# Kernel tuning notes

Measured on AMD Instinct MI355X. Metric: run time of the kernel, lower is better.

## Reference

```python
import jax, jax.numpy as jnp
import numpy as np

NUM_HEADS = 8
SIZES = [(80, 80), (40, 40), (20, 20), (10, 10), (5, 5)]


def _ln(x, g, b):
    m = x.mean(-1, keepdims=True)
    var = ((x - m) ** 2).mean(-1, keepdims=True)
    return (x - m) / jnp.sqrt(var + 1e-5) * g + b


def setup_inputs() -> dict:
    key = jax.random.key(0)
    ks = jax.random.split(key, 24)
    bs, c, S = 2, 256, 1024  # v_dim = embed_dim = c
    d = {}
    for i, (h, w) in enumerate(SIZES):
        d[f"q{i}"] = jax.random.normal(ks[i], (bs, c, h, w), jnp.float32)
    d["cache"] = jax.random.normal(ks[5], (bs, S, c), jnp.float32)
    d["mask"] = jax.random.randint(ks[6], (bs, S), 0, 2).astype(jnp.int32)
    d["ln_v_g"] = jnp.ones((c,), jnp.float32)
    d["ln_v_b"] = jnp.zeros((c,), jnp.float32)
    d["ln_c_g"] = jnp.ones((c,), jnp.float32)
    d["ln_c_b"] = jnp.zeros((c,), jnp.float32)
    sd = c ** -0.5
    d["Wv"] = jax.random.normal(ks[7], (c, c), jnp.float32) * sd
    d["bv"] = jnp.zeros((c,), jnp.float32)
    d["Wc"] = jax.random.normal(ks[8], (c, c), jnp.float32) * sd
    d["bc"] = jnp.zeros((c,), jnp.float32)
    d["Wvc"] = jax.random.normal(ks[9], (c, c), jnp.float32) * sd
    d["bvc"] = jnp.zeros((c,), jnp.float32)
    d["Wo"] = jax.random.normal(ks[10], (c, c), jnp.float32) * sd
    d["bo"] = jnp.zeros((c,), jnp.float32)
    d["Wg1"] = jax.random.normal(ks[11], (c, c // 2), jnp.float32) * sd
    d["bg1"] = jnp.zeros((c // 2,), jnp.float32)
    d["Wg2"] = jax.random.normal(ks[12], (c // 2, c), jnp.float32) * 0.01
    d["bg2"] = jnp.zeros((c,), jnp.float32)
    return d


def _forward(q0, q1, q2, q3, q4, cache, mask, ln_v_g, ln_v_b, ln_c_g, ln_c_b,
             Wv, bv, Wc, bc, Wvc, bvc, Wo, bo, Wg1, bg1, Wg2, bg2):
    feats = [q0, q1, q2, q3, q4]
    bs = q0.shape[0]
    sizes = [(f.shape[2], f.shape[3]) for f in feats]
    # permute_and_flatten: (bs, c, h, w) -> (bs, h*w, c), concat over levels
    v = jnp.concatenate(
        [f.reshape(bs, f.shape[1], -1).transpose(0, 2, 1) for f in feats], axis=1)
    T = v.shape[1]
    E = Wv.shape[1]
    hd = E // NUM_HEADS
    scale = hd ** -0.5

    vn = _ln(v, ln_v_g, ln_v_b)
    cn = _ln(cache, ln_c_g, ln_c_b)

    q = ((vn @ Wv + bv) * scale).reshape(bs, T, NUM_HEADS, hd).transpose(0, 2, 1, 3)
    k = (cn @ Wc + bc).reshape(bs, -1, NUM_HEADS, hd).transpose(0, 2, 1, 3)
    val = (cn @ Wvc + bvc).reshape(bs, -1, NUM_HEADS, hd).transpose(0, 2, 1, 3)

    attn = jnp.einsum('bhtd,bhsd->bhts', q, k)
    attn = jnp.clip(attn, -50000.0, 50000.0)
    mf = mask.astype(attn.dtype)  # (bs, S); zeros -> -9e15, ones kept as +1.0 (faithful)
    attn = attn + jnp.where(mf == 0, jnp.asarray(-9e15, attn.dtype), mf)[:, None, None, :]
    p = jax.nn.softmax(attn, axis=-1)  # dropout inactive in eval mode

    o = jnp.einsum('bhts,bhsd->bhtd', p, val).transpose(0, 2, 1, 3).reshape(bs, T, E)
    delta = o @ Wo + bo

    gate = jnp.tanh(jax.nn.relu(v @ Wg1 + bg1) @ Wg2 + bg2)
    new_v = (v + gate * delta).transpose(0, 2, 1)  # (bs, c, T)

    outs = []
    start = 0
    for h, w in sizes:
        outs.append(new_v[:, :, start:start + h * w].reshape(bs, -1, h, w))
        start += h * w
    return tuple(outs)


def reference(q0, q1, q2, q3, q4, cache, mask, ln_v_g, ln_v_b, ln_c_g, ln_c_b,
              Wv, bv, Wc, bc, Wvc, bvc, Wo, bo, Wg1, bg1, Wg2, bg2):
    return _forward(q0, q1, q2, q3, q4, cache, mask, ln_v_g, ln_v_b, ln_c_g, ln_c_b,
                    Wv, bv, Wc, bc, Wvc, bvc, Wo, bo, Wg1, bg1, Wg2, bg2)
```

## Files before the change

### kernel.cpp

```cpp
#include <hip/hip_runtime.h>
#include <hip/hip_bf16.h>
#include <math.h>


typedef __attribute__((ext_vector_type(8))) short short8;
typedef __attribute__((ext_vector_type(4))) float f32x4;
typedef __hip_bfloat16 bf16;

#define T_TOK 8525
#define S_TOK 1024
#define CDIM  256
#define NHEAD 8
#define BSZ   2

static __device__ __forceinline__ f32x4 mfma16(short8 a, short8 b, f32x4 c) {
  return __builtin_amdgcn_mfma_f32_16x16x32_bf16(a, b, c, 0, 0, 0);
}

static __device__ __forceinline__ float fexp2(float x) {
#if __has_builtin(__builtin_amdgcn_exp2f)
  return __builtin_amdgcn_exp2f(x);
#else
  return exp2f(x);
#endif
}

static __device__ __forceinline__ unsigned int pack_bf16(float a, float b) {
#if __has_builtin(__builtin_amdgcn_perm)
  return __builtin_amdgcn_perm(__float_as_uint(b), __float_as_uint(a), 0x07060302u);
#else
  return (__float_as_uint(a) >> 16) | (__float_as_uint(b) & 0xFFFF0000u);
#endif
}

__global__ __launch_bounds__(256) void stage1(
    const float* __restrict__ q0, const float* __restrict__ q1,
    const float* __restrict__ q2, const float* __restrict__ q3,
    const float* __restrict__ q4,
    const float* __restrict__ Wv, const float* __restrict__ Wc,
    const float* __restrict__ Wvc, const float* __restrict__ Wo,
    const float* __restrict__ Wg1, const float* __restrict__ Wg2,
    const float* __restrict__ bv, const float* __restrict__ bg1,
    const float* __restrict__ bc, const float* __restrict__ bvc,
    const float* __restrict__ cache, const float* __restrict__ ln_c_g,
    const float* __restrict__ ln_c_b, const float* __restrict__ ln_v_g,
    const float* __restrict__ ln_v_b,
    bf16* __restrict__ WqgT, bf16* __restrict__ WcvcT, bf16* __restrict__ WoT,
    bf16* __restrict__ Wg2T, float* __restrict__ biasCV,
    float* __restrict__ biasQG, bf16* __restrict__ cnb,
    float* __restrict__ vT, bf16* __restrict__ vb, bf16* __restrict__ vnb) {
  __shared__ float sm[4160];
  const int bid = blockIdx.x, tid = threadIdx.x;
  if (bid == 80) {
    biasCV[tid] = bc[tid];
    biasCV[tid + 256] = bvc[tid];
    biasQG[tid] = bv[tid];
    if (tid < 128) biasQG[256 + tid] = bg1[tid];
    return;
  }
  if (bid > 80 && bid < 593) {
    int lane = tid & 63;
    int row = (bid - 81) * 4 + (tid >> 6);
    const float* x = cache + (size_t)row * CDIM;
    float v0 = x[lane], v1 = x[lane + 64], v2 = x[lane + 128], v3 = x[lane + 192];
    float s = v0 + v1 + v2 + v3;
    float s2 = v0 * v0 + v1 * v1 + v2 * v2 + v3 * v3;
#pragma unroll
    for (int off = 1; off < 64; off <<= 1) {
      s += __shfl_xor(s, off);
      s2 += __shfl_xor(s2, off);
    }
    float mean = s * (1.f / 256.f);
    float var = s2 * (1.f / 256.f) - mean * mean;
    float rstd = rsqrtf(var + 1e-5f);
    bf16* y = cnb + (size_t)row * CDIM;
    y[lane] = __float2bfloat16((v0 - mean) * rstd * ln_c_g[lane] + ln_c_b[lane]);
    y[lane + 64] = __float2bfloat16((v1 - mean) * rstd * ln_c_g[lane + 64] + ln_c_b[lane + 64]);
    y[lane + 128] = __float2bfloat16((v2 - mean) * rstd * ln_c_g[lane + 128] + ln_c_b[lane + 128]);
    y[lane + 192] = __float2bfloat16((v3 - mean) * rstd * ln_c_g[lane + 192] + ln_c_b[lane + 192]);
    return;
  }
  if (bid < 80) {
    float (*tl)[65] = (float(*)[65])sm;
    const float* W; bf16* WT; int K, N, local;
    if (bid < 16)      { W = Wv;  WT = WqgT;           K = 256; N = 256; local = bid; }
    else if (bid < 32) { W = Wc;  WT = WcvcT;          K = 256; N = 256; local = bid - 16; }
    else if (bid < 48) { W = Wvc; WT = WcvcT + 65536;  K = 256; N = 256; local = bid - 32; }
    else if (bid < 64) { W = Wo;  WT = WoT;            K = 256; N = 256; local = bid - 48; }
    else if (bid < 72) { W = Wg1; WT = WqgT + 65536;   K = 256; N = 128; local = bid - 64; }
    else               { W = Wg2; WT = Wg2T;           K = 128; N = 256; local = bid - 72; }
    const int ktiles = K >> 6;
    const int K0 = (local % ktiles) * 64, N0 = (local / ktiles) * 64;
    const int kk = tid >> 4, n4 = (tid & 15) * 4;
#pragma unroll
    for (int i = 0; i < 4; ++i) {
      int k = kk + 16 * i;
      float4 w4 = *(const float4*)&W[(size_t)(K0 + k) * N + N0 + n4];
      tl[n4 + 0][k] = w4.x; tl[n4 + 1][k] = w4.y;
      tl[n4 + 2][k] = w4.z; tl[n4 + 3][k] = w4.w;
    }
    __syncthreads();
    const int nn = tid >> 4, k4 = (tid & 15) * 4;
#pragma unroll
    for (int i = 0; i < 4; ++i) {
      int n = nn + 16 * i;
      bf16 o[4] __attribute__((aligned(8)));
#pragma unroll
      for (int j = 0; j < 4; ++j) o[j] = __float2bfloat16(tl[n][k4 + j]);
      *(uint2*)&WT[(size_t)(N0 + n) * K + K0 + k4] = *(uint2*)o;
    }
    return;
  }
  constexpr int HW[5] = {6400, 1600, 400, 100, 25};
  constexpr int TST[5] = {0, 6400, 8000, 8400, 8500};
  constexpr int T16[5] = {0, 400, 500, 525, 532};
  float (*tile)[260] = (float(*)[260])sm;
  const int bb = bid - 593;
  const int tileid = bb % 534, b = bb / 534;
  int lvl = 0;
#pragma unroll
  for (int i = 1; i < 5; ++i) if (tileid >= T16[i]) lvl = i;
  const int p0 = (tileid - T16[lvl]) * 16;
  const int hw = HW[lvl];
  const float* src = ((lvl == 0) ? q0 : (lvl == 1) ? q1 : (lvl == 2) ? q2
                      : (lvl == 3) ? q3 : q4) + (size_t)b * CDIM * hw;
  const int pl = tid & 15, cb = tid >> 4;
  const int pg = p0 + pl;
#pragma unroll
  for (int i = 0; i < 16; ++i) {
    int c = cb + 16 * i;
    tile[pl][c] = (pg < hw) ? src[(size_t)c * hw + pg] : 0.f;
  }
  __syncthreads();
  if (pg < hw) {
    int tglob = TST[lvl] + pg;
#pragma unroll
    for (int i = 0; i < 16; ++i) {
      int c = cb + 16 * i;
      vT[((size_t)b * CDIM + c) * T_TOK + tglob] = tile[pl][c];
    }
  }
  const int lane = tid & 63, w = tid >> 6;
#pragma unroll
  for (int rr = 0; rr < 4; ++rr) {
    int row = w * 4 + rr;
    int p = p0 + row;
    if (p >= hw) continue;
    float x0 = tile[row][lane], x1 = tile[row][lane + 64],
          x2 = tile[row][lane + 128], x3 = tile[row][lane + 192];
    float s = x0 + x1 + x2 + x3;
    float s2 = x0 * x0 + x1 * x1 + x2 * x2 + x3 * x3;
#pragma unroll
    for (int off = 1; off < 64; off <<= 1) {
      s += __shfl_xor(s, off);
      s2 += __shfl_xor(s2, off);
    }
    float mean = s * (1.f / 256.f);
    float var = s2 * (1.f / 256.f) - mean * mean;
    float rstd = rsqrtf(var + 1e-5f);
    size_t base = ((size_t)b * T_TOK + TST[lvl] + p) * CDIM;
    float xs[4] = {x0, x1, x2, x3};
#pragma unroll
    for (int j = 0; j < 4; ++j) {
      int c = lane + 64 * j;
      float x = xs[j];
      vb[base + c] = __float2bfloat16(x);
      vnb[base + c] = __float2bfloat16((x - mean) * rstd * ln_v_g[c] + ln_v_b[c]);
    }
  }
}

__global__ __launch_bounds__(256) void gemm_qg(
    const bf16* __restrict__ vnb, const bf16* __restrict__ vb,
    const bf16* __restrict__ WqgT, const float* __restrict__ biasQG,
    bf16* __restrict__ qb, bf16* __restrict__ ghb, int M) {
  __shared__ __align__(16) bf16 Asl[128][136];
  __shared__ __align__(16) bf16 Bsl[64][136];
  const int tid = threadIdx.x;
  const int wave = tid >> 6, lane = tid & 63, quad = lane >> 4, l15 = lane & 15;
  const int m0 = blockIdx.y * 128;
  const int n0 = blockIdx.x * 64;
  const bf16* A = (n0 < 256) ? vnb : vb;
  f32x4 acc[2][4];
#pragma unroll
  for (int i = 0; i < 2; ++i)
#pragma unroll
    for (int j = 0; j < 4; ++j) acc[i][j] = (f32x4){0.f, 0.f, 0.f, 0.f};

  for (int k0 = 0; k0 < 256; k0 += 128) {
    __syncthreads();
#pragma unroll
    for (int c = 0; c < 8; ++c) {
      int chunk = c * 256 + tid;
      int row = chunk >> 4, col = (chunk & 15) * 8;
      int gr = m0 + row;
      if (gr >= M) gr = M - 1;
      *(uint4*)&Asl[row][col] = *(const uint4*)&A[(size_t)gr * 256 + k0 + col];
    }
#pragma unroll
    for (int c = 0; c < 4; ++c) {
      int chunk = c * 256 + tid;
      int row = chunk >> 4, col = (chunk & 15) * 8;
      *(uint4*)&Bsl[row][col] = *(const uint4*)&WqgT[(size_t)(n0 + row) * 256 + k0 + col];
    }
    __syncthreads();
#pragma unroll
    for (int kk = 0; kk < 128; kk += 32) {
      short8 af0 = *(const short8*)&Asl[wave * 32 + l15][kk + quad * 8];
      short8 af1 = *(const short8*)&Asl[wave * 32 + 16 + l15][kk + quad * 8];
      short8 bf0 = *(const short8*)&Bsl[l15][kk + quad * 8];
      short8 bf1 = *(const short8*)&Bsl[16 + l15][kk + quad * 8];
      short8 bf2 = *(const short8*)&Bsl[32 + l15][kk + quad * 8];
      short8 bf3 = *(const short8*)&Bsl[48 + l15][kk + quad * 8];
      acc[0][0] = mfma16(af0, bf0, acc[0][0]);
      acc[0][1] = mfma16(af0, bf1, acc[0][1]);
      acc[0][2] = mfma16(af0, bf2, acc[0][2]);
      acc[0][3] = mfma16(af0, bf3, acc[0][3]);
      acc[1][0] = mfma16(af1, bf0, acc[1][0]);
      acc[1][1] = mfma16(af1, bf1, acc[1][1]);
      acc[1][2] = mfma16(af1, bf2, acc[1][2]);
      acc[1][3] = mfma16(af1, bf3, acc[1][3]);
    }
  }
#pragma unroll
  for (int ms = 0; ms < 2; ++ms)
#pragma unroll
    for (int nt = 0; nt < 4; ++nt)
#pragma unroll
      for (int r = 0; r < 4; ++r) {
        int m = m0 + wave * 32 + ms * 16 + quad * 4 + r;
        if (m >= M) continue;
        int n = n0 + nt * 16 + l15;
        float x = acc[ms][nt][r] + biasQG[n];
        if (n < 256) {
          qb[(size_t)m * 256 + n] = __float2bfloat16(x * 0.25504765517f);
        } else {
          ghb[(size_t)m * 128 + (n - 256)] = __float2bfloat16(fmaxf(x, 0.f));
        }
      }
}

__global__ __launch_bounds__(256) void gemm_kval(
    const bf16* __restrict__ cnb, const bf16* __restrict__ WcvcT,
    const float* __restrict__ biasCV, bf16* __restrict__ kb,
    bf16* __restrict__ valTb, int M) {
  __shared__ __align__(16) bf16 Asl[128][136];
  __shared__ __align__(16) bf16 Bsl[64][136];
  const int tid = threadIdx.x;
  const int wave = tid >> 6, lane = tid & 63, quad = lane >> 4, l15 = lane & 15;
  const int m0 = blockIdx.y * 128;
  const int n0 = blockIdx.x * 64;
  f32x4 acc[2][4];
#pragma unroll
  for (int i = 0; i < 2; ++i)
#pragma unroll
    for (int j = 0; j < 4; ++j) acc[i][j] = (f32x4){0.f, 0.f, 0.f, 0.f};

  for (int k0 = 0; k0 < 256; k0 += 128) {
    __syncthreads();
#pragma unroll
    for (int c = 0; c < 8; ++c) {
      int chunk = c * 256 + tid;
      int row = chunk >> 4, col = (chunk & 15) * 8;
      *(uint4*)&Asl[row][col] = *(const uint4*)&cnb[(size_t)(m0 + row) * 256 + k0 + col];
    }
#pragma unroll
    for (int c = 0; c < 4; ++c) {
      int chunk = c * 256 + tid;
      int row = chunk >> 4, col = (chunk & 15) * 8;
      *(uint4*)&Bsl[row][col] = *(const uint4*)&WcvcT[(size_t)(n0 + row) * 256 + k0 + col];
    }
    __syncthreads();
#pragma unroll
    for (int kk = 0; kk < 128; kk += 32) {
      short8 af0 = *(const short8*)&Asl[wave * 32 + l15][kk + quad * 8];
      short8 af1 = *(const short8*)&Asl[wave * 32 + 16 + l15][kk + quad * 8];
      short8 bf0 = *(const short8*)&Bsl[l15][kk + quad * 8];
      short8 bf1 = *(const short8*)&Bsl[16 + l15][kk + quad * 8];
      short8 bf2 = *(const short8*)&Bsl[32 + l15][kk + quad * 8];
      short8 bf3 = *(const short8*)&Bsl[48 + l15][kk + quad * 8];
      acc[0][0] = mfma16(af0, bf0, acc[0][0]);
      acc[0][1] = mfma16(af0, bf1, acc[0][1]);
      acc[0][2] = mfma16(af0, bf2, acc[0][2]);
      acc[0][3] = mfma16(af0, bf3, acc[0][3]);
      acc[1][0] = mfma16(af1, bf0, acc[1][0]);
      acc[1][1] = mfma16(af1, bf1, acc[1][1]);
      acc[1][2] = mfma16(af1, bf2, acc[1][2]);
      acc[1][3] = mfma16(af1, bf3, acc[1][3]);
    }
  }
#pragma unroll
  for (int ms = 0; ms < 2; ++ms)
#pragma unroll
    for (int nt = 0; nt < 4; ++nt)
#pragma unroll
      for (int r = 0; r < 4; ++r) {
        int m = m0 + wave * 32 + ms * 16 + quad * 4 + r;
        int n = n0 + nt * 16 + l15;
        float x = acc[ms][nt][r] + biasCV[n];
        if (n < 256) {
          kb[(size_t)m * 256 + n] = __float2bfloat16(x);
        } else {
          int n2 = n - 256;
          int bb = m >> 10, s = m & 1023;
          int hh = n2 >> 5, d = n2 & 31;
          valTb[(((size_t)(bb * NHEAD + hh) * 32 + d) << 10) + s] = __float2bfloat16(x);
        }
      }
}

__global__ __launch_bounds__(512) void attn_kernel(
    const bf16* __restrict__ qb, const bf16* __restrict__ kb,
    const bf16* __restrict__ valTb, const int* __restrict__ mask,
    bf16* __restrict__ ob) {
  __shared__ __align__(16) bf16 Ksl[2][4096];
  __shared__ __align__(16) bf16 Vsl[2][4096];
  __shared__ __align__(16) float biasl[2][128];
  const int tid = threadIdx.x;
  const int lane = tid & 63, wv = tid >> 6, quad = lane >> 4, l15 = lane & 15;
  const int b = blockIdx.y >> 3, h = blockIdx.y & 7;
  const int t0w = blockIdx.x * 128 + wv * 16;
  int tA = t0w + l15;
  if (tA >= T_TOK) tA = T_TOK - 1;
  short8 qf = *(const short8*)&qb[((size_t)b * T_TOK + tA) * CDIM + h * 32 + quad * 8];
  f32x4 o0 = {0.f, 0.f, 0.f, 0.f};
  f32x4 o1 = {0.f, 0.f, 0.f, 0.f};
  f32x4 o2 = {0.f, 0.f, 0.f, 0.f};
  const short8 ones = (short8){0x3F80, 0x3F80, 0x3F80, 0x3F80,
                               0x3F80, 0x3F80, 0x3F80, 0x3F80};
  const size_t kbase = ((size_t)b * S_TOK) * CDIM + h * 32;
  const size_t vbase = (size_t)(b * NHEAD + h) << 15;
  const int ks = tid >> 2, kd16 = tid & 3;
  const int kdst = (ks >> 4) * 512 + (ks & 15) * 32 + kd16 * 8;
  const size_t kofs = (size_t)ks * CDIM + kd16 * 8;
  const int vd = tid >> 4, vs8 = (tid & 15) * 8;
  const int schunk = vs8 >> 5, sb_ = vs8 & 31;
  const int kb1 = (((sb_ >> 2) & 3) << 3) + (((sb_ >> 4) & 1) << 2);
  const int sb2_ = sb_ + 4;
  const int kb2 = (((sb2_ >> 2) & 3) << 3) + (((sb2_ >> 4) & 1) << 2);
  const int vbl = schunk * 1024 + (vd >> 4) * 512 + (vd & 15) * 32;
  const int vd1 = vbl + kb1, vd2 = vbl + kb2;
  const size_t vofs = ((size_t)vd << 10) + vs8;

  uint4 kreg = *(const uint4*)&kb[kbase + kofs];
  uint4 vreg = *(const uint4*)&valTb[vbase + vofs];
  float breg = 0.f;
  if (tid < 128) breg = mask[b * S_TOK + tid] ? -12.984255368f : -1e18f;
  *(uint4*)&Ksl[0][kdst] = kreg;
  {
    uint2 lo; lo.x = vreg.x; lo.y = vreg.y;
    uint2 hi; hi.x = vreg.z; hi.y = vreg.w;
    *(uint2*)&Vsl[0][vd1] = lo;
    *(uint2*)&Vsl[0][vd2] = hi;
  }
  if (tid < 128) biasl[0][tid] = breg;
  __syncthreads();

  for (int sbi = 0; sbi < 8; ++sbi) {
    const int cur = sbi & 1;
    if (sbi < 7) {
      int sb = (sbi + 1) * 128;
      kreg = *(const uint4*)&kb[kbase + (size_t)sb * CDIM + kofs];
      vreg = *(const uint4*)&valTb[vbase + sb + vofs];
      if (tid < 128) breg = mask[b * S_TOK + sb + tid] ? -12.984255368f : -1e18f;
    }
#pragma unroll
    for (int ss = 0; ss < 128; ss += 32) {
      const int cb = (ss >> 5) * 1024 + l15 * 32 + quad * 8;
      short8 kf0 = *(const short8*)&Ksl[cur][cb];
      short8 kf1 = *(const short8*)&Ksl[cur][cb + 512];
      short8 vf0 = *(const short8*)&Vsl[cur][cb];
      short8 vf1 = *(const short8*)&Vsl[cur][cb + 512];
      f32x4 bias0 = *(const f32x4*)&biasl[cur][ss + quad * 4];
      f32x4 bias1 = *(const f32x4*)&biasl[cur][ss + 16 + quad * 4];
      f32x4 s0 = mfma16(kf0, qf, bias0);
      f32x4 s1 = mfma16(kf1, qf, bias1);
      float pa = fexp2(s0[0]), pb = fexp2(s0[1]);
      float pc = fexp2(s0[2]), pd = fexp2(s0[3]);
      float pe = fexp2(s1[0]), pf_ = fexp2(s1[1]);
      float pg = fexp2(s1[2]), ph = fexp2(s1[3]);
      uint4 pu;
      pu.x = pack_bf16(pa, pb); pu.y = pack_bf16(pc, pd);
      pu.z = pack_bf16(pe, pf_); pu.w = pack_bf16(pg, ph);
      short8 pfr = *(short8*)&pu;
      o2 = mfma16(pfr, ones, o2);
      o0 = mfma16(pfr, vf0, o0);
      o1 = mfma16(pfr, vf1, o1);
    }
    if (sbi < 7) {
      const int nxt = cur ^ 1;
      *(uint4*)&Ksl[nxt][kdst] = kreg;
      uint2 lo; lo.x = vreg.x; lo.y = vreg.y;
      uint2 hi; hi.x = vreg.z; hi.y = vreg.w;
      *(uint2*)&Vsl[nxt][vd1] = lo;
      *(uint2*)&Vsl[nxt][vd2] = hi;
      if (tid < 128) biasl[nxt][tid] = breg;
    }
    __syncthreads();
  }
  bf16* tile = &Ksl[0][0] + wv * 512;
#pragma unroll
  for (int r = 0; r < 4; ++r) {
    float rli = 1.0f / o2[r];
    int tl = quad * 4 + r;
    tile[tl * 32 + l15] = __float2bfloat16(o0[r] * rli);
    tile[tl * 32 + 16 + l15] = __float2bfloat16(o1[r] * rli);
  }
  {
    int tl = lane >> 2;
    int d8 = (lane & 3) * 8;
    int t = t0w + tl;
    uint4 val = *(const uint4*)&tile[tl * 32 + d8];
    if (t < T_TOK)
      *(uint4*)&ob[((size_t)b * T_TOK + t) * CDIM + h * 32 + d8] = val;
  }
}

__global__ __launch_bounds__(256) void gemm_out(
    const bf16* __restrict__ obuf, const bf16* __restrict__ WoT,
    const float* __restrict__ bo, const bf16* __restrict__ ghb,
    const bf16* __restrict__ Wg2T, const float* __restrict__ bg2,
    const float* __restrict__ vT, float* __restrict__ out, int M) {
  constexpr int HW[5] = {6400, 1600, 400, 100, 25};
  constexpr int TST[5] = {0, 6400, 8000, 8400, 8500};
  constexpr size_t OUTOFF[5] = {0, 3276800, 4096000, 4300800, 4352000};
  __shared__ __align__(16) char smem[52224];
  bf16 (*Asl)[136] = (bf16(*)[136])smem;
  bf16 (*Bsl)[136] = (bf16(*)[136])(smem + 34816);
  float (*tile)[132] = (float(*)[132])smem;
  const int tid = threadIdx.x;
  const int wave = tid >> 6, lane = tid & 63, quad = lane >> 4, l15 = lane & 15;
  const int m0 = blockIdx.y * 128, n0 = blockIdx.x * 64;
  f32x4 aD[2][4], aG[2][4];
#pragma unroll
  for (int i = 0; i < 2; ++i)
#pragma unroll
    for (int j = 0; j < 4; ++j) {
      aD[i][j] = (f32x4){0.f, 0.f, 0.f, 0.f};
      aG[i][j] = (f32x4){0.f, 0.f, 0.f, 0.f};
    }
  for (int k0 = 0; k0 < 256; k0 += 128) {
    __syncthreads();
#pragma unroll
    for (int c = 0; c < 8; ++c) {
      int chunk = c * 256 + tid;
      int row = chunk >> 4, col = (chunk & 15) * 8;
      int gr = m0 + row;
      if (gr >= M) gr = M - 1;
      *(uint4*)&Asl[row][col] = *(const uint4*)&obuf[(size_t)gr * 256 + k0 + col];
    }
#pragma unroll
    for (int c = 0; c < 4; ++c) {
      int chunk = c * 256 + tid;
      int row = chunk >> 4, col = (chunk & 15) * 8;
      *(uint4*)&Bsl[row][col] = *(const uint4*)&WoT[(size_t)(n0 + row) * 256 + k0 + col];
    }
    __syncthreads();
#pragma unroll
    for (int kk = 0; kk < 128; kk += 32) {
      short8 af0 = *(const short8*)&Asl[wave * 32 + l15][kk + quad * 8];
      short8 af1 = *(const short8*)&Asl[wave * 32 + 16 + l15][kk + quad * 8];
#pragma unroll
      for (int j = 0; j < 4; ++j) {
        short8 bfj = *(const short8*)&Bsl[j * 16 + l15][kk + quad * 8];
        aD[0][j] = mfma16(af0, bfj, aD[0][j]);
        aD[1][j] = mfma16(af1, bfj, aD[1][j]);
      }
    }
  }
  __syncthreads();
#pragma unroll
  for (int c = 0; c < 8; ++c) {
    int chunk = c * 256 + tid;
    int row = chunk >> 4, col = (chunk & 15) * 8;
    int gr = m0 + row;
    if (gr >= M) gr = M - 1;
    *(uint4*)&Asl[row][col] = *(const uint4*)&ghb[(size_t)gr * 128 + col];
  }
#pragma unroll
  for (int c = 0; c < 4; ++c) {
    int chunk = c * 256 + tid;
    int row = chunk >> 4, col = (chunk & 15) * 8;
    *(uint4*)&Bsl[row][col] = *(const uint4*)&Wg2T[(size_t)(n0 + row) * 128 + col];
  }
  __syncthreads();
#pragma unroll
  for (int kk = 0; kk < 128; kk += 32) {
    short8 af0 = *(const short8*)&Asl[wave * 32 + l15][kk + quad * 8];
    short8 af1 = *(const short8*)&Asl[wave * 32 + 16 + l15][kk + quad * 8];
#pragma unroll
    for (int j = 0; j < 4; ++j) {
      short8 bfj = *(const short8*)&Bsl[j * 16 + l15][kk + quad * 8];
      aG[0][j] = mfma16(af0, bfj, aG[0][j]);
      aG[1][j] = mfma16(af1, bfj, aG[1][j]);
    }
  }
  __syncthreads();
#pragma unroll
  for (int ms = 0; ms < 2; ++ms)
#pragma unroll
    for (int nt = 0; nt < 4; ++nt) {
      int n = n0 + nt * 16 + l15;
      float bod = bo[n], bgd = bg2[n];
      float4 res;
      float tmp[4];
#pragma unroll
      for (int r = 0; r < 4; ++r) {
        float xd = aD[ms][nt][r] + bod;
        float xg = aG[ms][nt][r] + bgd;
        float xc = fminf(fmaxf(xg, -15.f), 15.f);
        float e = __expf(2.f * xc);
        float gt = (e - 1.f) / (e + 1.f);
        tmp[r] = gt * xd;
      }
      res.x = tmp[0]; res.y = tmp[1]; res.z = tmp[2]; res.w = tmp[3];
      *(float4*)&tile[nt * 16 + l15][wave * 32 + ms * 16 + quad * 4] = res;
    }
  __syncthreads();
  const int tl = tid & 127, c2 = tid >> 7;
  const int t = m0 + tl;
  const bool valid = t < M;
  int bb = (t >= T_TOK) ? 1 : 0;
  int tt = t - bb * T_TOK;
  if (tt >= T_TOK) tt = T_TOK - 1;
  int lvl = 0;
#pragma unroll
  for (int i = 1; i < 5; ++i) if (tt >= TST[i]) lvl = i;
  const int p = tt - TST[lvl], hw = HW[lvl];
  float* dst = out + OUTOFF[lvl] + ((size_t)bb * CDIM + n0) * hw + p;
  const float* vsrc = vT + ((size_t)bb * CDIM + n0) * T_TOK + tt;
#pragma unroll
  for (int c0 = 0; c0 < 32; ++c0) {
    int c = c0 * 2 + c2;
    if (valid) dst[(size_t)c * hw] = vsrc[(size_t)c * T_TOK] + tile[c][tl];
  }
}

extern "C" void kernel_launch(void* const* d_in, const int* in_sizes, int n_in,
                              void* d_out, int out_size, void* d_ws, size_t ws_size,
                              hipStream_t stream) {
  const float* q0 = (const float*)d_in[0];
  const float* q1 = (const float*)d_in[1];
  const float* q2 = (const float*)d_in[2];
  const float* q3 = (const float*)d_in[3];
  const float* q4 = (const float*)d_in[4];
  const float* cache = (const float*)d_in[5];
  const int* mask = (const int*)d_in[6];
  const float* ln_v_g = (const float*)d_in[7];
  const float* ln_v_b = (const float*)d_in[8];
  const float* ln_c_g = (const float*)d_in[9];
  const float* ln_c_b = (const float*)d_in[10];
  const float* Wv = (const float*)d_in[11];
  const float* bv = (const float*)d_in[12];
  const float* Wc = (const float*)d_in[13];
  const float* bc = (const float*)d_in[14];
  const float* Wvc = (const float*)d_in[15];
  const float* bvc = (const float*)d_in[16];
  const float* Wo = (const float*)d_in[17];
  const float* bo = (const float*)d_in[18];
  const float* Wg1 = (const float*)d_in[19];
  const float* bg1 = (const float*)d_in[20];
  const float* Wg2 = (const float*)d_in[21];
  const float* bg2 = (const float*)d_in[22];
  float* out = (float*)d_out;

  const int R = BSZ * T_TOK;
  const size_t RC = (size_t)R * CDIM;
  const size_t SC = (size_t)BSZ * S_TOK * CDIM;

  char* p = (char*)d_ws;
  float* vT = (float*)p;           p += RC * 4;
  bf16* vb = (bf16*)p;             p += RC * 2;
  bf16* vnb = (bf16*)p;            p += RC * 2;
  bf16* qb = (bf16*)p;             p += RC * 2;
  bf16* ob = (bf16*)p;             p += RC * 2;
  bf16* ghb = (bf16*)p;            p += (size_t)R * 128 * 2;
  bf16* cnb = (bf16*)p;            p += SC * 2;
  bf16* kb = (bf16*)p;             p += SC * 2;
  bf16* valTb = (bf16*)p;          p += SC * 2;
  bf16* WqgT = (bf16*)p;           p += 98304 * 2;
  bf16* WcvcT = (bf16*)p;          p += 131072 * 2;
  bf16* WoT = (bf16*)p;            p += 65536 * 2;
  bf16* Wg2T = (bf16*)p;           p += 32768 * 2;
  float* biasCV = (float*)p;       p += 512 * 4;
  float* biasQG = (float*)p;       p += 384 * 4;

  stage1<<<dim3(1661), dim3(256), 0, stream>>>(
      q0, q1, q2, q3, q4, Wv, Wc, Wvc, Wo, Wg1, Wg2, bv, bg1, bc, bvc,
      cache, ln_c_g, ln_c_b, ln_v_g, ln_v_b,
      WqgT, WcvcT, WoT, Wg2T, biasCV, biasQG, cnb, vT, vb, vnb);
  gemm_qg<<<dim3(6, 134), dim3(256), 0, stream>>>(
      vnb, vb, WqgT, biasQG, qb, ghb, R);
  gemm_kval<<<dim3(8, 16), dim3(256), 0, stream>>>(
      cnb, WcvcT, biasCV, kb, valTb, BSZ * S_TOK);
  attn_kernel<<<dim3(67, BSZ * NHEAD), dim3(512), 0, stream>>>(
      qb, kb, valTb, mask, ob);
  gemm_out<<<dim3(4, 134), dim3(256), 0, stream>>>(
      ob, WoT, bo, ghb, Wg2T, bg2, vT, out, R);
}
```

Before: 213.0 us.

## Merge QG and KV GEMMs into one launch, pre-pack mask, store residual as bf16

The two projection GEMMs become a single 1-D grid launch: the first 804 blocks compute Q and the gate hidden layer, the remaining blocks compute K and V. The mask is packed once in stage1 into 16-bit all-ones or zero pairs. The attention kernel now ANDs these masks onto the bf16 probabilities instead of staging a bias row in shared memory and adding it through the MFMA accumulator. The transposed residual copy of v is stored as bf16 rather than fp32, halving its write and read traffic, at the cost of residual precision in the final output. Dropping the constant exponent bias also changes how the exp values are scaled, which could raise overflow risk for large logits.

```diff
diff --git a/kernel.cpp b/kernel.cpp
--- a/kernel.cpp
+++ b/kernel.cpp
@@ -42,13 +42,14 @@
     const float* __restrict__ Wg1, const float* __restrict__ Wg2,
     const float* __restrict__ bv, const float* __restrict__ bg1,
     const float* __restrict__ bc, const float* __restrict__ bvc,
-    const float* __restrict__ cache, const float* __restrict__ ln_c_g,
-    const float* __restrict__ ln_c_b, const float* __restrict__ ln_v_g,
-    const float* __restrict__ ln_v_b,
+    const float* __restrict__ cache, const int* __restrict__ mask,
+    const float* __restrict__ ln_c_g, const float* __restrict__ ln_c_b,
+    const float* __restrict__ ln_v_g, const float* __restrict__ ln_v_b,
     bf16* __restrict__ WqgT, bf16* __restrict__ WcvcT, bf16* __restrict__ WoT,
     bf16* __restrict__ Wg2T, float* __restrict__ biasCV,
-    float* __restrict__ biasQG, bf16* __restrict__ cnb,
-    float* __restrict__ vT, bf16* __restrict__ vb, bf16* __restrict__ vnb) {
+    float* __restrict__ biasQG, unsigned int* __restrict__ mpk,
+    bf16* __restrict__ cnb, bf16* __restrict__ vTb,
+    bf16* __restrict__ vb, bf16* __restrict__ vnb) {
   __shared__ float sm[4160];
   const int bid = blockIdx.x, tid = threadIdx.x;
   if (bid == 80) {
@@ -56,6 +57,12 @@
     biasCV[tid + 256] = bvc[tid];
     biasQG[tid] = bv[tid];
     if (tid < 128) biasQG[256 + tid] = bg1[tid];
+#pragma unroll
+    for (int j = tid; j < 1024; j += 256) {
+      int bb = j >> 9, s2 = (j & 511) * 2;
+      mpk[j] = (mask[bb * 1024 + s2] ? 0xFFFFu : 0u) |
+               (mask[bb * 1024 + s2 + 1] ? 0xFFFF0000u : 0u);
+    }
     return;
   }
   if (bid > 80 && bid < 593) {
@@ -137,7 +144,7 @@
 #pragma unroll
     for (int i = 0; i < 16; ++i) {
       int c = cb + 16 * i;
-      vT[((size_t)b * CDIM + c) * T_TOK + tglob] = tile[pl][c];
+      vTb[((size_t)b * CDIM + c) * T_TOK + tglob] = __float2bfloat16(tile[pl][c]);
     }
   }
   const int lane = tid & 63, w = tid >> 6;
@@ -170,17 +177,30 @@
   }
 }
 
-__global__ __launch_bounds__(256) void gemm_qg(
+__global__ __launch_bounds__(256) void gemm_fused(
     const bf16* __restrict__ vnb, const bf16* __restrict__ vb,
     const bf16* __restrict__ WqgT, const float* __restrict__ biasQG,
-    bf16* __restrict__ qb, bf16* __restrict__ ghb, int M) {
+    bf16* __restrict__ qb, bf16* __restrict__ ghb,
+    const bf16* __restrict__ cnb, const bf16* __restrict__ WcvcT,
+    const float* __restrict__ biasCV, bf16* __restrict__ kb,
+    bf16* __restrict__ valTb) {
   __shared__ __align__(16) bf16 Asl[128][136];
   __shared__ __align__(16) bf16 Bsl[64][136];
   const int tid = threadIdx.x;
   const int wave = tid >> 6, lane = tid & 63, quad = lane >> 4, l15 = lane & 15;
-  const int m0 = blockIdx.y * 128;
-  const int n0 = blockIdx.x * 64;
-  const bf16* A = (n0 < 256) ? vnb : vb;
+  const int bid = blockIdx.x;
+  const bool kval = bid >= 804;
+  int m0, n0, M;
+  const bf16 *A, *BW;
+  const float* bias;
+  if (!kval) {
+    m0 = (bid / 6) * 128; n0 = (bid % 6) * 64;
+    A = (n0 < 256) ? vnb : vb; BW = WqgT; bias = biasQG; M = BSZ * T_TOK;
+  } else {
+    int i = bid - 804;
+    m0 = (i / 8) * 128; n0 = (i % 8) * 64;
+    A = cnb; BW = WcvcT; bias = biasCV; M = BSZ * S_TOK;
+  }
   f32x4 acc[2][4];
 #pragma unroll
   for (int i = 0; i < 2; ++i)
@@ -201,7 +221,7 @@
     for (int c = 0; c < 4; ++c) {
       int chunk = c * 256 + tid;
       int row = chunk >> 4, col = (chunk & 15) * 8;
-      *(uint4*)&Bsl[row][col] = *(const uint4*)&WqgT[(size_t)(n0 + row) * 256 + k0 + col];
+      *(uint4*)&Bsl[row][col] = *(const uint4*)&BW[(size_t)(n0 + row) * 256 + k0 + col];
     }
     __syncthreads();
 #pragma unroll
@@ -231,91 +251,32 @@
         int m = m0 + wave * 32 + ms * 16 + quad * 4 + r;
         if (m >= M) continue;
         int n = n0 + nt * 16 + l15;
-        float x = acc[ms][nt][r] + biasQG[n];
-        if (n < 256) {
-          qb[(size_t)m * 256 + n] = __float2bfloat16(x * 0.25504765517f);
+        float x = acc[ms][nt][r] + bias[n];
+        if (!kval) {
+          if (n < 256) {
+            qb[(size_t)m * 256 + n] = __float2bfloat16(x * 0.25504765517f);
+          } else {
+            ghb[(size_t)m * 128 + (n - 256)] = __float2bfloat16(fmaxf(x, 0.f));
+          }
         } else {
-          ghb[(size_t)m * 128 + (n - 256)] = __float2bfloat16(fmaxf(x, 0.f));
+          if (n < 256) {
+            kb[(size_t)m * 256 + n] = __float2bfloat16(x);
+          } else {
+            int n2 = n - 256;
+            int bb = m >> 10, s = m & 1023;
+            int hh = n2 >> 5, d = n2 & 31;
+            valTb[(((size_t)(bb * NHEAD + hh) * 32 + d) << 10) + s] = __float2bfloat16(x);
+          }
         }
       }
 }
 
-__global__ __launch_bounds__(256) void gemm_kval(
-    const bf16* __restrict__ cnb, const bf16* __restrict__ WcvcT,
-    const float* __restrict__ biasCV, bf16* __restrict__ kb,
-    bf16* __restrict__ valTb, int M) {
-  __shared__ __align__(16) bf16 Asl[128][136];
-  __shared__ __align__(16) bf16 Bsl[64][136];
-  const int tid = threadIdx.x;
-  const int wave = tid >> 6, lane = tid & 63, quad = lane >> 4, l15 = lane & 15;
-  const int m0 = blockIdx.y * 128;
-  const int n0 = blockIdx.x * 64;
-  f32x4 acc[2][4];
-#pragma unroll
-  for (int i = 0; i < 2; ++i)
-#pragma unroll
-    for (int j = 0; j < 4; ++j) acc[i][j] = (f32x4){0.f, 0.f, 0.f, 0.f};
-
-  for (int k0 = 0; k0 < 256; k0 += 128) {
-    __syncthreads();
-#pragma unroll
-    for (int c = 0; c < 8; ++c) {
-      int chunk = c * 256 + tid;
-      int row = chunk >> 4, col = (chunk & 15) * 8;
-      *(uint4*)&Asl[row][col] = *(const uint4*)&cnb[(size_t)(m0 + row) * 256 + k0 + col];
-    }
-#pragma unroll
-    for (int c = 0; c < 4; ++c) {
-      int chunk = c * 256 + tid;
-      int row = chunk >> 4, col = (chunk & 15) * 8;
-      *(uint4*)&Bsl[row][col] = *(const uint4*)&WcvcT[(size_t)(n0 + row) * 256 + k0 + col];
-    }
-    __syncthreads();
-#pragma unroll
-    for (int kk = 0; kk < 128; kk += 32) {
-      short8 af0 = *(const short8*)&Asl[wave * 32 + l15][kk + quad * 8];
-      short8 af1 = *(const short8*)&Asl[wave * 32 + 16 + l15][kk + quad * 8];
-      short8 bf0 = *(const short8*)&Bsl[l15][kk + quad * 8];
-      short8 bf1 = *(const short8*)&Bsl[16 + l15][kk + quad * 8];
-      short8 bf2 = *(const short8*)&Bsl[32 + l15][kk + quad * 8];
-      short8 bf3 = *(const short8*)&Bsl[48 + l15][kk + quad * 8];
-      acc[0][0] = mfma16(af0, bf0, acc[0][0]);
-      acc[0][1] = mfma16(af0, bf1, acc[0][1]);
-      acc[0][2] = mfma16(af0, bf2, acc[0][2]);
-      acc[0][3] = mfma16(af0, bf3, acc[0][3]);
-      acc[1][0] = mfma16(af1, bf0, acc[1][0]);
-      acc[1][1] = mfma16(af1, bf1, acc[1][1]);
-      acc[1][2] = mfma16(af1, bf2, acc[1][2]);
-      acc[1][3] = mfma16(af1, bf3, acc[1][3]);
-    }
-  }
-#pragma unroll
-  for (int ms = 0; ms < 2; ++ms)
-#pragma unroll
-    for (int nt = 0; nt < 4; ++nt)
-#pragma unroll
-      for (int r = 0; r < 4; ++r) {
-        int m = m0 + wave * 32 + ms * 16 + quad * 4 + r;
-        int n = n0 + nt * 16 + l15;
-        float x = acc[ms][nt][r] + biasCV[n];
-        if (n < 256) {
-          kb[(size_t)m * 256 + n] = __float2bfloat16(x);
-        } else {
-          int n2 = n - 256;
-          int bb = m >> 10, s = m & 1023;
-          int hh = n2 >> 5, d = n2 & 31;
-          valTb[(((size_t)(bb * NHEAD + hh) * 32 + d) << 10) + s] = __float2bfloat16(x);
-        }
-      }
-}
-
 __global__ __launch_bounds__(512) void attn_kernel(
     const bf16* __restrict__ qb, const bf16* __restrict__ kb,
-    const bf16* __restrict__ valTb, const int* __restrict__ mask,
+    const bf16* __restrict__ valTb, const unsigned int* __restrict__ mpk,
     bf16* __restrict__ ob) {
   __shared__ __align__(16) bf16 Ksl[2][4096];
   __shared__ __align__(16) bf16 Vsl[2][4096];
-  __shared__ __align__(16) float biasl[2][128];
   const int tid = threadIdx.x;
   const int lane = tid & 63, wv = tid >> 6, quad = lane >> 4, l15 = lane & 15;
   const int b = blockIdx.y >> 3, h = blockIdx.y & 7;
@@ -326,10 +287,12 @@
   f32x4 o0 = {0.f, 0.f, 0.f, 0.f};
   f32x4 o1 = {0.f, 0.f, 0.f, 0.f};
   f32x4 o2 = {0.f, 0.f, 0.f, 0.f};
+  const f32x4 zero4 = {0.f, 0.f, 0.f, 0.f};
   const short8 ones = (short8){0x3F80, 0x3F80, 0x3F80, 0x3F80,
                                0x3F80, 0x3F80, 0x3F80, 0x3F80};
   const size_t kbase = ((size_t)b * S_TOK) * CDIM + h * 32;
   const size_t vbase = (size_t)(b * NHEAD + h) << 15;
+  const unsigned int* mrow = mpk + b * 512;
   const int ks = tid >> 2, kd16 = tid & 3;
   const int kdst = (ks >> 4) * 512 + (ks & 15) * 32 + kd16 * 8;
   const size_t kofs = (size_t)ks * CDIM + kd16 * 8;
@@ -344,8 +307,6 @@
 
   uint4 kreg = *(const uint4*)&kb[kbase + kofs];
   uint4 vreg = *(const uint4*)&valTb[vbase + vofs];
-  float breg = 0.f;
-  if (tid < 128) breg = mask[b * S_TOK + tid] ? -12.984255368f : -1e18f;
   *(uint4*)&Ksl[0][kdst] = kreg;
   {
     uint2 lo; lo.x = vreg.x; lo.y = vreg.y;
@@ -353,7 +314,6 @@
     *(uint2*)&Vsl[0][vd1] = lo;
     *(uint2*)&Vsl[0][vd2] = hi;
   }
-  if (tid < 128) biasl[0][tid] = breg;
   __syncthreads();
 
   for (int sbi = 0; sbi < 8; ++sbi) {
@@ -362,8 +322,8 @@
       int sb = (sbi + 1) * 128;
       kreg = *(const uint4*)&kb[kbase + (size_t)sb * CDIM + kofs];
       vreg = *(const uint4*)&valTb[vbase + sb + vofs];
-      if (tid < 128) breg = mask[b * S_TOK + sb + tid] ? -12.984255368f : -1e18f;
-    }
+    }
+    const unsigned int* mchunk = mrow + sbi * 64;
 #pragma unroll
     for (int ss = 0; ss < 128; ss += 32) {
       const int cb = (ss >> 5) * 1024 + l15 * 32 + quad * 8;
@@ -371,17 +331,19 @@
       short8 kf1 = *(const short8*)&Ksl[cur][cb + 512];
       short8 vf0 = *(const short8*)&Vsl[cur][cb];
       short8 vf1 = *(const short8*)&Vsl[cur][cb + 512];
-      f32x4 bias0 = *(const f32x4*)&biasl[cur][ss + quad * 4];
-      f32x4 bias1 = *(const f32x4*)&biasl[cur][ss + 16 + quad * 4];
-      f32x4 s0 = mfma16(kf0, qf, bias0);
-      f32x4 s1 = mfma16(kf1, qf, bias1);
+      uint2 mk0 = *(const uint2*)&mchunk[(ss >> 1) + quad * 2];
+      uint2 mk1 = *(const uint2*)&mchunk[(ss >> 1) + 8 + quad * 2];
+      f32x4 s0 = mfma16(kf0, qf, zero4);
+      f32x4 s1 = mfma16(kf1, qf, zero4);
       float pa = fexp2(s0[0]), pb = fexp2(s0[1]);
       float pc = fexp2(s0[2]), pd = fexp2(s0[3]);
       float pe = fexp2(s1[0]), pf_ = fexp2(s1[1]);
       float pg = fexp2(s1[2]), ph = fexp2(s1[3]);
       uint4 pu;
-      pu.x = pack_bf16(pa, pb); pu.y = pack_bf16(pc, pd);
-      pu.z = pack_bf16(pe, pf_); pu.w = pack_bf16(pg, ph);
+      pu.x = pack_bf16(pa, pb) & mk0.x;
+      pu.y = pack_bf16(pc, pd) & mk0.y;
+      pu.z = pack_bf16(pe, pf_) & mk1.x;
+      pu.w = pack_bf16(pg, ph) & mk1.y;
       short8 pfr = *(short8*)&pu;
       o2 = mfma16(pfr, ones, o2);
       o0 = mfma16(pfr, vf0, o0);
@@ -394,7 +356,6 @@
       uint2 hi; hi.x = vreg.z; hi.y = vreg.w;
       *(uint2*)&Vsl[nxt][vd1] = lo;
       *(uint2*)&Vsl[nxt][vd2] = hi;
-      if (tid < 128) biasl[nxt][tid] = breg;
     }
     __syncthreads();
   }
@@ -420,7 +381,7 @@
     const bf16* __restrict__ obuf, const bf16* __restrict__ WoT,
     const float* __restrict__ bo, const bf16* __restrict__ ghb,
     const bf16* __restrict__ Wg2T, const float* __restrict__ bg2,
-    const float* __restrict__ vT, float* __restrict__ out, int M) {
+    const bf16* __restrict__ vTb, float* __restrict__ out, int M) {
   constexpr int HW[5] = {6400, 1600, 400, 100, 25};
   constexpr int TST[5] = {0, 6400, 8000, 8400, 8500};
   constexpr size_t OUTOFF[5] = {0, 3276800, 4096000, 4300800, 4352000};
@@ -528,11 +489,12 @@
   for (int i = 1; i < 5; ++i) if (tt >= TST[i]) lvl = i;
   const int p = tt - TST[lvl], hw = HW[lvl];
   float* dst = out + OUTOFF[lvl] + ((size_t)bb * CDIM + n0) * hw + p;
-  const float* vsrc = vT + ((size_t)bb * CDIM + n0) * T_TOK + tt;
+  const bf16* vsrc = vTb + ((size_t)bb * CDIM + n0) * T_TOK + tt;
 #pragma unroll
   for (int c0 = 0; c0 < 32; ++c0) {
     int c = c0 * 2 + c2;
-    if (valid) dst[(size_t)c * hw] = vsrc[(size_t)c * T_TOK] + tile[c][tl];
+    if (valid)
+      dst[(size_t)c * hw] = __bfloat162float(vsrc[(size_t)c * T_TOK]) + tile[c][tl];
   }
 }
 
@@ -569,7 +531,7 @@
   const size_t SC = (size_t)BSZ * S_TOK * CDIM;
 
   char* p = (char*)d_ws;
-  float* vT = (float*)p;           p += RC * 4;
+  bf16* vTb = (bf16*)p;            p += RC * 2;
   bf16* vb = (bf16*)p;             p += RC * 2;
   bf16* vnb = (bf16*)p;            p += RC * 2;
   bf16* qb = (bf16*)p;             p += RC * 2;
@@ -584,17 +546,16 @@
   bf16* Wg2T = (bf16*)p;           p += 32768 * 2;
   float* biasCV = (float*)p;       p += 512 * 4;
   float* biasQG = (float*)p;       p += 384 * 4;
+  unsigned int* mpk = (unsigned int*)p; p += 1024 * 4;
 
   stage1<<<dim3(1661), dim3(256), 0, stream>>>(
       q0, q1, q2, q3, q4, Wv, Wc, Wvc, Wo, Wg1, Wg2, bv, bg1, bc, bvc,
-      cache, ln_c_g, ln_c_b, ln_v_g, ln_v_b,
-      WqgT, WcvcT, WoT, Wg2T, biasCV, biasQG, cnb, vT, vb, vnb);
-  gemm_qg<<<dim3(6, 134), dim3(256), 0, stream>>>(
-      vnb, vb, WqgT, biasQG, qb, ghb, R);
-  gemm_kval<<<dim3(8, 16), dim3(256), 0, stream>>>(
-      cnb, WcvcT, biasCV, kb, valTb, BSZ * S_TOK);
+      cache, mask, ln_c_g, ln_c_b, ln_v_g, ln_v_b,
+      WqgT, WcvcT, WoT, Wg2T, biasCV, biasQG, mpk, cnb, vTb, vb, vnb);
+  gemm_fused<<<dim3(932), dim3(256), 0, stream>>>(
+      vnb, vb, WqgT, biasQG, qb, ghb, cnb, WcvcT, biasCV, kb, valTb);
   attn_kernel<<<dim3(67, BSZ * NHEAD), dim3(512), 0, stream>>>(
-      qb, kb, valTb, mask, ob);
+      qb, kb, valTb, mpk, ob);
   gemm_out<<<dim3(4, 134), dim3(256), 0, stream>>>(
-      ob, WoT, bo, ghb, Wg2T, bg2, vT, out, R);
-}
+      ob, WoT, bo, ghb, Wg2T, bg2, vTb, out, R);
+}
```

New measurement: 205.9 us. 3.3% less time.
